# Kernel optimization log

Hardware: AMD Instinct MI355X
Metric: run time of the kernel (lower is better)

Reference implementation:

```python
import jax, jax.numpy as jnp
import numpy as np

HEADS = 8
DIM_HEAD = 64

def setup_inputs() -> dict:
    key = jax.random.key(0)
    k1, k2 = jax.random.split(key)
    x = jax.random.normal(k1, (4, 2048, 512), dtype=jnp.float32)
    W_qkv = jax.random.normal(k2, (512, 3 * HEADS * DIM_HEAD), dtype=jnp.float32) * (512 ** -0.5)
    return {"x": x, "W_qkv": W_qkv}

def reference(x, W_qkv):
    b, n, _ = x.shape
    h, d = HEADS, DIM_HEAD
    scale = d ** -0.5
    qkv = x @ W_qkv                                   # [b, n, 3*h*d]
    q, k, v = jnp.split(qkv, 3, axis=-1)
    # 'b n (h d) -> b h n d'
    q = q.reshape(b, n, h, d).transpose(0, 2, 1, 3)
    k = k.reshape(b, n, h, d).transpose(0, 2, 1, 3)
    v = v.reshape(b, n, h, d).transpose(0, 2, 1, 3)
    scores = jnp.einsum('bhid,bhjd->bhij', q, k) * scale
    attn_w = jax.nn.softmax(scores, axis=-1)
    out = jnp.einsum('bhij,bhjd->bhid', attn_w, v)
    # 'b h i d -> b i (h d)'
    return out.transpose(0, 2, 1, 3).reshape(b, n, h * d)
```

## Files before the change

kernel.cpp:

```cpp
#include <hip/hip_runtime.h>

#define BATCH 4
#define NSEQ  2048
#define DMODEL 512
#define NHEAD 8
#define DHEAD 64
#define NQKV  1536

typedef __bf16 bf16x8 __attribute__((ext_vector_type(8)));
typedef __bf16 bf16x4 __attribute__((ext_vector_type(4)));
typedef float  f32x4  __attribute__((ext_vector_type(4)));
typedef short  s16x4  __attribute__((ext_vector_type(4)));

__device__ inline void async16(const __bf16* g, __bf16* l) {
    __builtin_amdgcn_global_load_lds(
        (const __attribute__((address_space(1))) void*)g,
        (__attribute__((address_space(3))) void*)l, 16, 0, 0);
}

__device__ inline f32x4 mfma_pv(s16x4 a, s16x4 b, f32x4 c) {
#if !defined(__HIP_DEVICE_COMPILE__)
    (void)a; (void)b;
    return c;
#elif __has_builtin(__builtin_amdgcn_mfma_f32_16x16x16bf16_1k)
    return __builtin_amdgcn_mfma_f32_16x16x16bf16_1k(a, b, c, 0, 0, 0);
#else
    bf16x4 a4 = __builtin_bit_cast(bf16x4, a);
    bf16x4 b4 = __builtin_bit_cast(bf16x4, b);
    bf16x8 a8 = {}, b8 = {};
    for (int i = 0; i < 4; ++i) { a8[i] = a4[i]; b8[i] = b4[i]; }
    return __builtin_amdgcn_mfma_f32_16x16x32_bf16(a8, b8, c, 0, 0, 0);
#endif
}

#define QSCALE 0.18033688011112042f

__global__ __launch_bounds__(256) void prep_kernel(
    const float* __restrict__ x, const float* __restrict__ W,
    __bf16* __restrict__ xb, __bf16* __restrict__ Wt) {
    __shared__ __bf16 t[64][65];
    const int tid = threadIdx.x;
    if (blockIdx.x < 4096) {
        int idx = blockIdx.x * 256 + tid;
        float4 v = ((const float4*)x)[idx];
        bf16x4 o = {(__bf16)v.x, (__bf16)v.y, (__bf16)v.z, (__bf16)v.w};
        ((bf16x4*)xb)[idx] = o;
        return;
    }
    const int bi = blockIdx.x - 4096;
    const int n0 = (bi % 24) * 64, k0 = (bi / 24) * 64;
    const int cr = tid >> 4;
    const int cc = (tid & 15) * 4;
    for (int p = 0; p < 4; ++p) {
        int r = p * 16 + cr;
        float4 v = *(const float4*)&W[(size_t)(k0 + r) * NQKV + n0 + cc];
        t[r][cc + 0] = (__bf16)v.x; t[r][cc + 1] = (__bf16)v.y;
        t[r][cc + 2] = (__bf16)v.z; t[r][cc + 3] = (__bf16)v.w;
    }
    __syncthreads();
    for (int p = 0; p < 4; ++p) {
        int r = p * 16 + cr;
        bf16x4 o = {t[cc + 0][r], t[cc + 1][r], t[cc + 2][r], t[cc + 3][r]};
        *(bf16x4*)&Wt[(size_t)(n0 + r) * DMODEL + k0 + cc] = o;
    }
}

__global__ __launch_bounds__(256) void qkv_gemm_kernel(
    const __bf16* __restrict__ xb, const __bf16* __restrict__ Wt,
    __bf16* __restrict__ Qw, __bf16* __restrict__ Kw, __bf16* __restrict__ Vw) {
    __shared__ __align__(16) char smem[128 * 136 * 2];
    __bf16* Al = (__bf16*)smem;
    __bf16* Bl = Al + 8192;
    __bf16* T  = (__bf16*)smem;

    const int tid  = threadIdx.x;
    const int w    = tid >> 6;
    const int lane = tid & 63;
    const int quad = lane >> 4;
    const int l15  = lane & 15;
    const int wm   = w >> 1, wn = w & 1;
    const int m0 = blockIdx.x * 128;
    const int n0 = blockIdx.y * 128;
    const int segrow = lane >> 3;
    const int sc = (lane & 7) ^ segrow;

    f32x4 acc[4][4];
    for (int i = 0; i < 4; ++i)
        for (int j = 0; j < 4; ++j)
            acc[i][j] = (f32x4){0.f, 0.f, 0.f, 0.f};

    for (int kt = 0; kt < 8; ++kt) {
        const int k0 = kt * 64;
        for (int i = 0; i < 4; ++i) {
            int seg = w * 4 + i;
            int row = seg * 8 + segrow;
            async16(&xb[(size_t)(m0 + row) * DMODEL + k0 + sc * 8], &Al[seg * 512]);
            async16(&Wt[(size_t)(n0 + row) * DMODEL + k0 + sc * 8], &Bl[seg * 512]);
        }
        __syncthreads();
        for (int kc = 0; kc < 2; ++kc) {
            bf16x8 af[4], bfr[4];
            for (int mb = 0; mb < 4; ++mb) {
                int row = wm * 64 + mb * 16 + l15;
                af[mb] = *(const bf16x8*)&Al[row * 64 + (((kc * 4 + quad) ^ (l15 & 7)) * 8)];
            }
            for (int nb = 0; nb < 4; ++nb) {
                int row = wn * 64 + nb * 16 + l15;
                bfr[nb] = *(const bf16x8*)&Bl[row * 64 + (((kc * 4 + quad) ^ (l15 & 7)) * 8)];
            }
            for (int mb = 0; mb < 4; ++mb)
                for (int nb = 0; nb < 4; ++nb)
                    acc[mb][nb] = __builtin_amdgcn_mfma_f32_16x16x32_bf16(
                        af[mb], bfr[nb], acc[mb][nb], 0, 0, 0);
        }
        __syncthreads();
    }

    const int which = n0 >> 9;
    const int bb  = m0 >> 11;
    const int nq0 = m0 & 2047;

    if (which <= 1) {
        for (int mb = 0; mb < 4; ++mb)
            for (int nb = 0; nb < 4; ++nb)
                for (int r = 0; r < 4; ++r) {
                    int ml = wm * 64 + mb * 16 + quad * 4 + r;
                    int nl = wn * 64 + nb * 16 + l15;
                    float a = acc[mb][nb][r];
                    if (which == 0) a *= QSCALE;
                    T[ml * 136 + nl] = (__bf16)a;
                }
        __syncthreads();
        __bf16* dst = which ? Kw : Qw;
        const int h0 = (n0 & 511) >> 6;
        const int region = tid >> 7;
        const int bh = bb * NHEAD + h0 + region;
        __bf16* base = dst + ((size_t)bh * NSEQ + nq0) * DHEAD;
        for (int i = 0; i < 8; ++i) {
            int chunk = (tid & 127) + i * 128;
            int f = chunk * 8;
            int ml = f >> 6, dd = f & 63;
            bf16x8 v = *(const bf16x8*)&T[ml * 136 + region * 64 + dd];
            *(bf16x8*)&base[ml * 64 + dd] = v;
        }
    } else {
        for (int mb = 0; mb < 4; ++mb)
            for (int nb = 0; nb < 4; ++nb) {
                int nl = wn * 64 + nb * 16 + l15;
                int mlb = wm * 64 + mb * 16 + quad * 4;
                bf16x4 v = {(__bf16)acc[mb][nb][0], (__bf16)acc[mb][nb][1],
                            (__bf16)acc[mb][nb][2], (__bf16)acc[mb][nb][3]};
                *(bf16x4*)&T[nl * 136 + mlb] = v;
            }
        __syncthreads();
        const int hv0 = ((n0 - 1024) & 511) >> 6;
        for (int i = 0; i < 8; ++i) {
            int gc = i * 256 + tid;
            int row = gc >> 4, ch = gc & 15;
            bf16x8 v = *(const bf16x8*)&T[row * 136 + ch * 8];
            int bh = bb * NHEAD + hv0 + (row >> 6);
            int dd = row & 63;
            *(bf16x8*)&Vw[((size_t)bh * DHEAD + dd) * NSEQ + nq0 + ch * 8] = v;
        }
    }
}

__global__ __launch_bounds__(512) void attn_kernel(
    const __bf16* __restrict__ Qw, const __bf16* __restrict__ Kw,
    const __bf16* __restrict__ Vw, float* __restrict__ out) {
    __shared__ __align__(16) char smem[128 * 68 * 4];
    __bf16* Kl = (__bf16*)smem;
    __bf16* Vl = Kl + 8192;
    float*  Of = (float*)smem;

    const int tid  = threadIdx.x;
    const int w    = tid >> 6;
    const int lane = tid & 63;
    const int quad = lane >> 4;
    const int l15  = lane & 15;
    const int bh = blockIdx.y;
    const int bb = bh >> 3, h = bh & 7;
    const int q0 = blockIdx.x * 128 + w * 16;
    const int segrow = lane >> 3;
    const int sc = (lane & 7) ^ segrow;

    const __bf16* Qh = Qw + (size_t)bh * NSEQ * DHEAD;
    const __bf16* Kh = Kw + (size_t)bh * NSEQ * DHEAD;
    const __bf16* Vh = Vw + (size_t)bh * DHEAD * NSEQ;

    bf16x8 qf[2];
    for (int kc = 0; kc < 2; ++kc)
        qf[kc] = *(const bf16x8*)&Qh[(size_t)(q0 + l15) * DHEAD + kc * 32 + quad * 8];

    f32x4 O[4];
    float l_st = 0.f;
    for (int db = 0; db < 4; ++db)
        O[db] = (f32x4){0.f, 0.f, 0.f, 0.f};

    auto stage = [&](int kt, int b) {
        const int k0 = kt * 64;
        int row = w * 8 + segrow;
        async16(&Kh[(size_t)(k0 + row) * DHEAD + sc * 8], &Kl[b * 4096 + w * 512]);
        async16(&Vh[(size_t)row * NSEQ + k0 + sc * 8], &Vl[b * 4096 + w * 512]);
    };

    stage(0, 0);
    for (int kt = 0; kt < 32; ++kt) {
        __syncthreads();
        if (kt < 31) stage(kt + 1, (kt + 1) & 1);
        const __bf16* Kb = Kl + (kt & 1) * 4096;
        const __bf16* Vb = Vl + (kt & 1) * 4096;

        f32x4 s[4];
        for (int kb = 0; kb < 4; ++kb)
            s[kb] = (f32x4){0.f, 0.f, 0.f, 0.f};
        for (int kc = 0; kc < 2; ++kc) {
            bf16x8 ak[4];
            for (int kb = 0; kb < 4; ++kb) {
                int row = kb * 16 + l15;
                ak[kb] = *(const bf16x8*)&Kb[row * 64 + (((kc * 4 + quad) ^ (l15 & 7)) * 8)];
            }
            for (int kb = 0; kb < 4; ++kb)
                s[kb] = __builtin_amdgcn_mfma_f32_16x16x32_bf16(
                    ak[kb], qf[kc], s[kb], 0, 0, 0);
        }

        s16x4 pb[4];
        float rsum = 0.f;
        for (int kb = 0; kb < 4; ++kb) {
            bf16x4 t;
            for (int r = 0; r < 4; ++r) {
                float p = __builtin_amdgcn_exp2f(s[kb][r]);
                rsum += p;
                t[r] = (__bf16)p;
            }
            pb[kb] = __builtin_bit_cast(s16x4, t);
        }
        rsum += __shfl_xor(rsum, 16);
        rsum += __shfl_xor(rsum, 32);
        l_st += rsum;

        for (int kb = 0; kb < 4; ++kb) {
            s16x4 av[4];
            for (int db = 0; db < 4; ++db) {
                int d = db * 16 + l15;
                int g = kb * 2 + (quad >> 1);
                av[db] = *(const s16x4*)&Vb[(d >> 3) * 512 + (d & 7) * 64 +
                                            ((g ^ (d & 7)) * 8) + (quad & 1) * 4];
            }
            for (int db = 0; db < 4; ++db)
                O[db] = mfma_pv(av[db], pb[kb], O[db]);
        }
    }

    __syncthreads();
    {
        float inv = 1.f / l_st;
        int q = w * 16 + l15;
        for (int db = 0; db < 4; ++db) {
            f32x4 v = O[db] * inv;
            *(f32x4*)&Of[q * 68 + db * 16 + quad * 4] = v;
        }
    }
    __syncthreads();
    const int nqb = blockIdx.x * 128;
    for (int i = 0; i < 4; ++i) {
        int gc = i * 512 + tid;
        int row = gc >> 4, ch = gc & 15;
        f32x4 v = *(const f32x4*)&Of[row * 68 + ch * 4];
        *(f32x4*)&out[((size_t)(bb * NSEQ + nqb + row)) * DMODEL + h * DHEAD + ch * 4] = v;
    }
}

extern "C" void kernel_launch(void* const* d_in, const int* in_sizes, int n_in,
                              void* d_out, int out_size, void* d_ws, size_t ws_size,
                              hipStream_t stream) {
    const float* x = (const float*)d_in[0];
    const float* W = (const float*)d_in[1];
    float* out = (float*)d_out;

    __bf16* wsp = (__bf16*)d_ws;
    __bf16* xb = wsp;
    __bf16* Wt = xb + 4194304;
    __bf16* Qw = Wt + 786432;
    __bf16* Kw = Qw + 4194304;
    __bf16* Vw = Kw + 4194304;

    prep_kernel<<<4288, 256, 0, stream>>>(x, W, xb, Wt);
    qkv_gemm_kernel<<<dim3(64, 12), 256, 0, stream>>>(xb, Wt, Qw, Kw, Vw);
    attn_kernel<<<dim3(16, 32), 512, 0, stream>>>(Qw, Kw, Vw, out);
}
```

Baseline: 147.5 us.

## Split KV range across wave halves and process two query tiles per wave

Each wave now handles 32 queries as two 16-row tiles, so every K/V fragment read from LDS feeds two MFMAs instead of one. To keep all 128 queries covered, the 8 waves form two halves that each walk half of the key sequence into their own LDS buffer. The halves' partial outputs and row sums are merged through LDS at the end. In exchange, the double-buffered prefetch is dropped: each tile is loaded, then a barrier, then compute, so load latency is no longer hidden. Some K/V segments are also loaded twice, and register pressure rises.

```diff
diff --git a/kernel.cpp b/kernel.cpp
--- a/kernel.cpp
+++ b/kernel.cpp
@@ -169,97 +169,122 @@
     const __bf16* __restrict__ Qw, const __bf16* __restrict__ Kw,
     const __bf16* __restrict__ Vw, float* __restrict__ out) {
     __shared__ __align__(16) char smem[128 * 68 * 4];
-    __bf16* Kl = (__bf16*)smem;
-    __bf16* Vl = Kl + 8192;
-    float*  Of = (float*)smem;
+    float* Of = (float*)smem;
 
     const int tid  = threadIdx.x;
     const int w    = tid >> 6;
+    const int wg   = w & 3;
+    const int half = w >> 2;
     const int lane = tid & 63;
     const int quad = lane >> 4;
     const int l15  = lane & 15;
     const int bh = blockIdx.y;
     const int bb = bh >> 3, h = bh & 7;
-    const int q0 = blockIdx.x * 128 + w * 16;
+    const int q0 = blockIdx.x * 128 + wg * 32;
     const int segrow = lane >> 3;
     const int sc = (lane & 7) ^ segrow;
+
+    __bf16* KL = (__bf16*)(smem + half * 16384);
+    __bf16* VL = KL + 4096;
 
     const __bf16* Qh = Qw + (size_t)bh * NSEQ * DHEAD;
     const __bf16* Kh = Kw + (size_t)bh * NSEQ * DHEAD;
     const __bf16* Vh = Vw + (size_t)bh * DHEAD * NSEQ;
 
-    bf16x8 qf[2];
-    for (int kc = 0; kc < 2; ++kc)
-        qf[kc] = *(const bf16x8*)&Qh[(size_t)(q0 + l15) * DHEAD + kc * 32 + quad * 8];
-
-    f32x4 O[4];
-    float l_st = 0.f;
+    bf16x8 qf[2][2];
+    for (int qb = 0; qb < 2; ++qb)
+        for (int kc = 0; kc < 2; ++kc)
+            qf[qb][kc] = *(const bf16x8*)&Qh[(size_t)(q0 + qb * 16 + l15) * DHEAD + kc * 32 + quad * 8];
+
+    f32x4 O[4][2];
+    float l_st[2] = {0.f, 0.f};
     for (int db = 0; db < 4; ++db)
-        O[db] = (f32x4){0.f, 0.f, 0.f, 0.f};
-
-    auto stage = [&](int kt, int b) {
-        const int k0 = kt * 64;
-        int row = w * 8 + segrow;
-        async16(&Kh[(size_t)(k0 + row) * DHEAD + sc * 8], &Kl[b * 4096 + w * 512]);
-        async16(&Vh[(size_t)row * NSEQ + k0 + sc * 8], &Vl[b * 4096 + w * 512]);
-    };
-
-    stage(0, 0);
-    for (int kt = 0; kt < 32; ++kt) {
-        __syncthreads();
-        if (kt < 31) stage(kt + 1, (kt + 1) & 1);
-        const __bf16* Kb = Kl + (kt & 1) * 4096;
-        const __bf16* Vb = Vl + (kt & 1) * 4096;
-
-        f32x4 s[4];
+        for (int qb = 0; qb < 2; ++qb)
+            O[db][qb] = (f32x4){0.f, 0.f, 0.f, 0.f};
+
+    for (int it = 0; it < 16; ++it) {
+        const int k0 = (half * 16 + it) * 64;
+        for (int i = 0; i < 2; ++i) {
+            int seg = wg * 2 + i;
+            int row = seg * 8 + segrow;
+            async16(&Kh[(size_t)(k0 + row) * DHEAD + sc * 8], &KL[seg * 512]);
+            async16(&Vh[(size_t)row * NSEQ + k0 + sc * 8], &VL[seg * 512]);
+            seg += 8 - wg * 2;
+        }
+        {
+            int seg = 4 + wg;
+            int row = seg * 8 + segrow;
+            async16(&Kh[(size_t)(k0 + row) * DHEAD + sc * 8], &KL[seg * 512]);
+            async16(&Vh[(size_t)row * NSEQ + k0 + sc * 8], &VL[seg * 512]);
+        }
+        __syncthreads();
+
+        f32x4 s[4][2];
         for (int kb = 0; kb < 4; ++kb)
-            s[kb] = (f32x4){0.f, 0.f, 0.f, 0.f};
+            for (int qb = 0; qb < 2; ++qb)
+                s[kb][qb] = (f32x4){0.f, 0.f, 0.f, 0.f};
         for (int kc = 0; kc < 2; ++kc) {
             bf16x8 ak[4];
             for (int kb = 0; kb < 4; ++kb) {
                 int row = kb * 16 + l15;
-                ak[kb] = *(const bf16x8*)&Kb[row * 64 + (((kc * 4 + quad) ^ (l15 & 7)) * 8)];
+                ak[kb] = *(const bf16x8*)&KL[row * 64 + (((kc * 4 + quad) ^ (l15 & 7)) * 8)];
             }
             for (int kb = 0; kb < 4; ++kb)
-                s[kb] = __builtin_amdgcn_mfma_f32_16x16x32_bf16(
-                    ak[kb], qf[kc], s[kb], 0, 0, 0);
-        }
-
-        s16x4 pb[4];
-        float rsum = 0.f;
-        for (int kb = 0; kb < 4; ++kb) {
-            bf16x4 t;
-            for (int r = 0; r < 4; ++r) {
-                float p = __builtin_amdgcn_exp2f(s[kb][r]);
-                rsum += p;
-                t[r] = (__bf16)p;
-            }
-            pb[kb] = __builtin_bit_cast(s16x4, t);
-        }
-        rsum += __shfl_xor(rsum, 16);
-        rsum += __shfl_xor(rsum, 32);
-        l_st += rsum;
+                for (int qb = 0; qb < 2; ++qb)
+                    s[kb][qb] = __builtin_amdgcn_mfma_f32_16x16x32_bf16(
+                        ak[kb], qf[qb][kc], s[kb][qb], 0, 0, 0);
+        }
+
+        s16x4 pb[4][2];
+        for (int qb = 0; qb < 2; ++qb) {
+            float rsum = 0.f;
+            for (int kb = 0; kb < 4; ++kb) {
+                bf16x4 t;
+                for (int r = 0; r < 4; ++r) {
+                    float p = __builtin_amdgcn_exp2f(s[kb][qb][r]);
+                    rsum += p;
+                    t[r] = (__bf16)p;
+                }
+                pb[kb][qb] = __builtin_bit_cast(s16x4, t);
+            }
+            rsum += __shfl_xor(rsum, 16);
+            rsum += __shfl_xor(rsum, 32);
+            l_st[qb] += rsum;
+        }
 
         for (int kb = 0; kb < 4; ++kb) {
             s16x4 av[4];
             for (int db = 0; db < 4; ++db) {
                 int d = db * 16 + l15;
                 int g = kb * 2 + (quad >> 1);
-                av[db] = *(const s16x4*)&Vb[(d >> 3) * 512 + (d & 7) * 64 +
+                av[db] = *(const s16x4*)&VL[(d >> 3) * 512 + (d & 7) * 64 +
                                             ((g ^ (d & 7)) * 8) + (quad & 1) * 4];
             }
             for (int db = 0; db < 4; ++db)
-                O[db] = mfma_pv(av[db], pb[kb], O[db]);
-        }
-    }
-
+                for (int qb = 0; qb < 2; ++qb)
+                    O[db][qb] = mfma_pv(av[db], pb[kb][qb], O[db][qb]);
+        }
+        __syncthreads();
+    }
+
+    if (half == 0) {
+        for (int qb = 0; qb < 2; ++qb) {
+            int q = wg * 32 + qb * 16 + l15;
+            for (int db = 0; db < 4; ++db)
+                *(f32x4*)&Of[q * 68 + db * 16 + quad * 4] = O[db][qb];
+            if (quad == 0) Of[q * 68 + 64] = l_st[qb];
+        }
+    }
     __syncthreads();
-    {
-        float inv = 1.f / l_st;
-        int q = w * 16 + l15;
-        for (int db = 0; db < 4; ++db) {
-            f32x4 v = O[db] * inv;
-            *(f32x4*)&Of[q * 68 + db * 16 + quad * 4] = v;
+    if (half == 1) {
+        for (int qb = 0; qb < 2; ++qb) {
+            int q = wg * 32 + qb * 16 + l15;
+            float inv = 1.f / (l_st[qb] + Of[q * 68 + 64]);
+            for (int db = 0; db < 4; ++db) {
+                f32x4 v = *(const f32x4*)&Of[q * 68 + db * 16 + quad * 4];
+                v = (v + O[db][qb]) * inv;
+                *(f32x4*)&Of[q * 68 + db * 16 + quad * 4] = v;
+            }
         }
     }
     __syncthreads();
```

Result: no change. 148.6 us (+0.8%).
